# Performance work log

Hardware: AMD Instinct MI355X
Metric: run time of the kernel (lower is better)

## Reference

```python
import jax, jax.numpy as jnp
import numpy as np

# ---- constants matching init_kwargs ----
Z_RES_LIST = (1, 2, 4, 64)
Z_MAX = 64.0
HC = 2                      # heatmap_xy_coeff
PAD = 3 * HC                # xy patch half-width = 6; patch size 13
PATCH = 2 * PAD + 1         # 13
SIZE = 64
BATCH, JOINTS = 16, 17
# heatmap_z_coeff = 2*floor((6*HC*z_res/z_max + 1)/2) + 1 -> [1, 1, 1, 13]
Z_COEFFS = tuple(int(2 * np.floor((6 * HC * zr / Z_MAX + 1) / 2) + 1) for zr in Z_RES_LIST)


def gaussian_3d(size, depth, sigma=0.25, mean=0.5, amplitude=1.0):
    mean_u = mean * size + 0.5
    mean_r = mean * depth + 0.5
    over_s = 1.0 / (sigma * size)
    over_r = 1.0 / (sigma * depth)
    x = jnp.arange(size, dtype=jnp.float32)
    z = jnp.arange(depth, dtype=jnp.float32)
    du = (x + 1 - mean_u) * over_s          # [size] (same for u and v since square)
    dr = (z + 1 - mean_r) * over_r          # [depth]
    return amplitude * jnp.exp(-0.5 * (du[None, None, :] ** 2
                                       + du[None, :, None] ** 2
                                       + dr[:, None, None] ** 2))  # [depth, size, size]


def _level_voxel(coords, g, z_res, z_coeff):
    """Vectorized equivalent of the per-(b,j) slice-copy: the patch g (centered at
    (zidx, y, x), zero outside) is written into a zero [B,J,z_res,SIZE,SIZE] grid."""
    zpad = z_coeff // 2
    zidx = (jnp.ceil(coords[:, :, 2] * z_res / Z_MAX) - 1).astype(jnp.int32)  # [B,J]
    xi = coords[:, :, 0].astype(jnp.int32)  # trunc like .short(); coords >= 0
    yi = coords[:, :, 1].astype(jnp.int32)
    # patch-space indices for every voxel coordinate
    gz = jnp.arange(z_res)[None, None, :] - zidx[:, :, None] + zpad   # [B,J,Z]
    gy = jnp.arange(SIZE)[None, None, :] - yi[:, :, None] + PAD       # [B,J,S]
    gx = jnp.arange(SIZE)[None, None, :] - xi[:, :, None] + PAD       # [B,J,S]
    vz = (gz >= 0) & (gz < z_coeff)
    vy = (gy >= 0) & (gy < PATCH)
    vx = (gx >= 0) & (gx < PATCH)
    gzc = jnp.clip(gz, 0, z_coeff - 1)
    gyc = jnp.clip(gy, 0, PATCH - 1)
    gxc = jnp.clip(gx, 0, PATCH - 1)
    vals = g[gzc[:, :, :, None, None], gyc[:, :, None, :, None], gxc[:, :, None, None, :]]
    valid = vz[:, :, :, None, None] & vy[:, :, None, :, None] & vx[:, :, None, None, :]
    return jnp.where(valid, vals, jnp.float32(0.0))  # [B,J,z_res,SIZE,SIZE]


def setup_inputs() -> dict:
    key = jax.random.key(0)
    coords = jax.random.randint(key, (BATCH, JOINTS, 3), 0, 64).astype(jnp.float32)
    g0, g1, g2, g3 = (gaussian_3d(PATCH, zc) for zc in Z_COEFFS)
    return {"coords": coords, "g0": g0, "g1": g1, "g2": g2, "g3": g3}


def reference(coords, g0, g1, g2, g3):
    gs = (g0, g1, g2, g3)
    return tuple(_level_voxel(coords, g, zr, zc)
                 for g, zr, zc in zip(gs, Z_RES_LIST, Z_COEFFS))
```

## Files before the change

kernel.cpp:

```cpp
#include <hip/hip_runtime.h>


#define B_J 272
#define SIZE2 4096
#define PAD 6
#define PATCH 13
#define PP 169

__global__ __launch_bounds__(256)
void GaussianVoxel_scatter(const float* __restrict__ coords,
                           const float* __restrict__ g0,
                           const float* __restrict__ g1,
                           const float* __restrict__ g2,
                           const float* __restrict__ g3,
                           float* __restrict__ out) {
    const int bj = blockIdx.x;
    const int xi = (int)coords[bj * 3 + 0];
    const int yi = (int)coords[bj * 3 + 1];
    const int zi = (int)coords[bj * 3 + 2];

    const int        zrs[4]  = {1, 2, 4, 64};
    const int        zcs[4]  = {1, 1, 1, 13};
    const float*     gs[4]   = {g0, g1, g2, g3};
    const long long  offs[4] = {0LL, 1114112LL, 3342336LL, 7798784LL};

    for (int L = 0; L < 4; ++L) {
        const int zr   = zrs[L];
        const int zc   = zcs[L];
        const int zpad = zc >> 1;
        const int zidx = (zi * zr + 63) / 64 - 1;

        float* __restrict__ ob = out + offs[L] + (long long)bj * zr * SIZE2;
        const float* __restrict__ g = gs[L];

        const int total = zc * PP;
        for (int t = threadIdx.x; t < total; t += blockDim.x) {
            const int gz  = t / PP;
            const int rem = t - gz * PP;
            const int gy  = rem / PATCH;
            const int gx  = rem - gy * PATCH;
            const int zo  = zidx - zpad + gz;
            const int yo  = yi - PAD + gy;
            const int xo  = xi - PAD + gx;
            if ((unsigned)zo < (unsigned)zr &&
                (unsigned)yo < 64u &&
                (unsigned)xo < 64u) {
                ob[zo * SIZE2 + yo * 64 + xo] = g[t];
            }
        }
    }
}

extern "C" void kernel_launch(void* const* d_in, const int* in_sizes, int n_in,
                              void* d_out, int out_size, void* d_ws, size_t ws_size,
                              hipStream_t stream) {
    const float* coords = (const float*)d_in[0];
    const float* g0     = (const float*)d_in[1];
    const float* g1     = (const float*)d_in[2];
    const float* g2     = (const float*)d_in[3];
    const float* g3     = (const float*)d_in[4];
    float* out = (float*)d_out;

    hipMemsetAsync(out, 0, (size_t)out_size * sizeof(float), stream);

    GaussianVoxel_scatter<<<B_J, 256, 0, stream>>>(coords, g0, g1, g2, g3, out);
}
```

Baseline: 323.3 us.

## Fuse zero-fill into a gather kernel writing every output slice with float4 stores

Drops the separate full-output memset and the scatter kernel. One block now produces each (b,j,z) 64x64 slice: it writes zeros directly when the slice is outside the patch, and otherwise gathers Gaussian values into vectorized float4 stores. Each output byte is written exactly once, with coalesced stores and no second kernel, at the cost of per-element bounds checks and a much larger grid.

```diff
diff --git a/kernel.cpp b/kernel.cpp
--- a/kernel.cpp
+++ b/kernel.cpp
@@ -1,53 +1,69 @@
 #include <hip/hip_runtime.h>
 
 
-#define B_J 272
-#define SIZE2 4096
 #define PAD 6
 #define PATCH 13
 #define PP 169
 
 __global__ __launch_bounds__(256)
-void GaussianVoxel_scatter(const float* __restrict__ coords,
-                           const float* __restrict__ g0,
-                           const float* __restrict__ g1,
-                           const float* __restrict__ g2,
-                           const float* __restrict__ g3,
-                           float* __restrict__ out) {
-    const int bj = blockIdx.x;
+void GaussianVoxel_fused(const float* __restrict__ coords,
+                         const float* __restrict__ g0,
+                         const float* __restrict__ g1,
+                         const float* __restrict__ g2,
+                         const float* __restrict__ g3,
+                         float* __restrict__ out) {
+    const int s = blockIdx.x;
+
+    int base, zsh;
+    long long obase;
+    const float* g;
+    if (s < 272)       { base = 0;    zsh = 0; obase = 0LL;       g = g0; }
+    else if (s < 816)  { base = 272;  zsh = 1; obase = 1114112LL; g = g1; }
+    else if (s < 1904) { base = 816;  zsh = 2; obase = 3342336LL; g = g2; }
+    else               { base = 1904; zsh = 6; obase = 7798784LL; g = g3; }
+    const int sid = s - base;
+    const int bj  = sid >> zsh;
+    const int z   = sid & ((1 << zsh) - 1);
+    const int zc   = (zsh == 6) ? 13 : 1;
+    const int zpad = (zsh == 6) ? 6  : 0;
+
+    float4* __restrict__ o4 = (float4*)(out + obase + (long long)sid * 4096);
+
     const int xi = (int)coords[bj * 3 + 0];
     const int yi = (int)coords[bj * 3 + 1];
     const int zi = (int)coords[bj * 3 + 2];
 
-    const int        zrs[4]  = {1, 2, 4, 64};
-    const int        zcs[4]  = {1, 1, 1, 13};
-    const float*     gs[4]   = {g0, g1, g2, g3};
-    const long long  offs[4] = {0LL, 1114112LL, 3342336LL, 7798784LL};
+    const int zidx = (((zi << zsh) + 63) >> 6) - 1;
+    const int gz = z - zidx + zpad;
 
-    for (int L = 0; L < 4; ++L) {
-        const int zr   = zrs[L];
-        const int zc   = zcs[L];
-        const int zpad = zc >> 1;
-        const int zidx = (zi * zr + 63) / 64 - 1;
+    const float4 zero = make_float4(0.f, 0.f, 0.f, 0.f);
 
-        float* __restrict__ ob = out + offs[L] + (long long)bj * zr * SIZE2;
-        const float* __restrict__ g = gs[L];
+    if ((unsigned)gz >= (unsigned)zc) {
+        #pragma unroll
+        for (int i = 0; i < 4; ++i)
+            o4[i * 256 + threadIdx.x] = zero;
+        return;
+    }
 
-        const int total = zc * PP;
-        for (int t = threadIdx.x; t < total; t += blockDim.x) {
-            const int gz  = t / PP;
-            const int rem = t - gz * PP;
-            const int gy  = rem / PATCH;
-            const int gx  = rem - gy * PATCH;
-            const int zo  = zidx - zpad + gz;
-            const int yo  = yi - PAD + gy;
-            const int xo  = xi - PAD + gx;
-            if ((unsigned)zo < (unsigned)zr &&
-                (unsigned)yo < 64u &&
-                (unsigned)xo < 64u) {
-                ob[zo * SIZE2 + yo * 64 + xo] = g[t];
+    const float* __restrict__ gsl = g + gz * PP;
+    #pragma unroll
+    for (int i = 0; i < 4; ++i) {
+        const int f4 = i * 256 + threadIdx.x;
+        const int e  = f4 << 2;
+        const int y  = e >> 6;
+        const int x  = e & 63;
+        const int gy = y - yi + PAD;
+        float4 v = zero;
+        if ((unsigned)gy < (unsigned)PATCH) {
+            const float* row = gsl + gy * PATCH;
+            #pragma unroll
+            for (int k = 0; k < 4; ++k) {
+                const int gx = x + k - xi + PAD;
+                if ((unsigned)gx < (unsigned)PATCH)
+                    ((float*)&v)[k] = row[gx];
             }
         }
+        o4[f4] = v;
     }
 }
 
@@ -61,7 +77,5 @@
     const float* g3     = (const float*)d_in[4];
     float* out = (float*)d_out;
 
-    hipMemsetAsync(out, 0, (size_t)out_size * sizeof(float), stream);
-
-    GaussianVoxel_scatter<<<B_J, 256, 0, stream>>>(coords, g0, g1, g2, g3, out);
+    GaussianVoxel_fused<<<19312, 256, 0, stream>>>(coords, g0, g1, g2, g3, out);
 }
```

Result: no change. 323.6 us (+0.1%).
